# Kernel optimization log

Hardware: AMD Instinct MI355X
Metric: run time of the kernel (lower is better)

Reference implementation:

```python
import jax, jax.numpy as jnp
import numpy as np

B, T, L, D, H, E, A, V = 64, 20, 196, 512, 512, 512, 512, 30000


def setup_inputs() -> dict:
    key = jax.random.key(0)
    ks = jax.random.split(key, 20)
    s = 0.02  # param init scale
    inp = {
        "captions": jax.random.randint(ks[0], (B, T), 0, V),
        "image_features": jax.random.normal(ks[1], (B, L, D), dtype=jnp.float32),
        "pooled_features": jax.random.normal(ks[2], (B, H), dtype=jnp.float32),
        "attention_mask": jnp.ones((B, L), dtype=bool),
        # embedding table
        "embedding": jax.random.normal(ks[3], (V, E), dtype=jnp.float32) * s,
        # LSTM (torch gate order i, f, g, o), input = [emb; context]
        "W_ih": jax.random.normal(ks[4], (4 * H, E + H), dtype=jnp.float32) * s,
        "W_hh": jax.random.normal(ks[5], (4 * H, H), dtype=jnp.float32) * s,
        "b_lstm": jnp.zeros((4 * H,), dtype=jnp.float32),
        # additive attention with memory/cell extra query context
        "Wq": jax.random.normal(ks[6], (H, A), dtype=jnp.float32) * s,
        "Wk": jax.random.normal(ks[7], (D, A), dtype=jnp.float32) * s,
        "Wm": jax.random.normal(ks[8], (H, A), dtype=jnp.float32) * s,
        "Wc": jax.random.normal(ks[9], (H, A), dtype=jnp.float32) * s,
        "v_att": jax.random.normal(ks[10], (A,), dtype=jnp.float32) * s,
        # output projection context(H) -> vocab
        "W_out": jax.random.normal(ks[11], (H, V), dtype=jnp.float32) * s,
        "b_out": jnp.zeros((V,), dtype=jnp.float32),
        # hidden/cell init from pooled features (num_layers = 1)
        "W_init_h": jax.random.normal(ks[12], (H, H), dtype=jnp.float32) * s,
        "b_init_h": jnp.zeros((H,), dtype=jnp.float32),
        "W_init_c": jax.random.normal(ks[13], (H, H), dtype=jnp.float32) * s,
        "b_init_c": jnp.zeros((H,), dtype=jnp.float32),
    }
    return inp


def reference(captions, image_features, pooled_features, attention_mask,
              embedding, W_ih, W_hh, b_lstm, Wq, Wk, Wm, Wc, v_att,
              W_out, b_out, W_init_h, b_init_h, W_init_c, b_init_c):
    # init hidden states from pooled features
    h0 = pooled_features @ W_init_h + b_init_h            # [B, H]
    c0 = pooled_features @ W_init_c + b_init_c            # [B, H]
    ctx0 = jnp.zeros_like(h0)                              # prev_context, [B, H]
    emb = embedding[captions]                              # [B, T, E] (dropout = eval identity)
    # precompute key projection once (hoisted out of the timestep loop)
    key_proj = jnp.einsum('bld,da->bla', image_features, Wk)  # [B, L, A]
    neg = jnp.finfo(image_features.dtype).min

    def step(carry, emb_t):
        h, c, ctx = carry
        x = jnp.concatenate([emb_t, ctx], axis=-1)         # [B, E+H]
        gates = x @ W_ih.T + h @ W_hh.T + b_lstm           # [B, 4H]
        i, f, g, o = jnp.split(gates, 4, axis=-1)
        i = jax.nn.sigmoid(i); f = jax.nn.sigmoid(f)
        g = jnp.tanh(g);       o = jax.nn.sigmoid(o)
        c_new = f * c + i * g
        h_new = o * jnp.tanh(c_new)                        # lstm output == query
        # additive attention: query + memory_state(h) + cell_state(c) context
        q = h_new @ Wq + h_new @ Wm + c_new @ Wc           # [B, A]
        scores = jnp.einsum('bla,a->bl', jnp.tanh(key_proj + q[:, None, :]), v_att)
        scores = jnp.where(attention_mask, scores, neg)
        w = jax.nn.softmax(scores, axis=-1)                # [B, L]
        ctx_new = jnp.einsum('bl,bld->bd', w, image_features)  # [B, H]
        logits_t = ctx_new @ W_out + b_out                 # [B, V]
        return (h_new, c_new, ctx_new), logits_t

    _, logits = jax.lax.scan(step, (h0, c0, ctx0), jnp.swapaxes(emb, 0, 1))
    return jnp.swapaxes(logits, 0, 1)  # [B, T, V]
```

## Files before the change

kernel.cpp:

```cpp
#include <hip/hip_runtime.h>
#include <hip/hip_bf16.h>
#include <cstdint>

#define DEV static __device__ __forceinline__

typedef __bf16 bf16;
typedef __bf16 bf16x8 __attribute__((ext_vector_type(8)));
typedef float f32x4 __attribute__((ext_vector_type(4)));

#define B_ 64
#define T_ 20
#define L_ 196
#define E_ 512
#define V_ 30000
#define VPAD 30080
#define XK 2560
#define GN 2048
#define KSPLIT 8
#define KSPAN 10

DEV float sigmoidf_(float x) { return 1.0f / (1.0f + __expf(-x)); }
DEV float tanhf_(float x) { float e = __expf(2.0f * x); return 1.0f - 2.0f / (e + 1.0f); }

DEV float ldf(const void* p, size_t i, int isbf) {
  return isbf ? (float)((const bf16*)p)[i] : ((const float*)p)[i];
}

DEV void gload_lds16(const void* g, void* l) {
  __builtin_amdgcn_global_load_lds(
      (const __attribute__((address_space(1))) void*)(uintptr_t)g,
      (__attribute__((address_space(3))) void*)(uint32_t)(uintptr_t)l,
      16, 0, 0);
}

#define WAITV4_BAR  do { asm volatile("s_waitcnt vmcnt(4)" ::: "memory"); \
                         asm volatile("s_barrier" ::: "memory"); } while (0)
#define WAITV2_BAR  do { asm volatile("s_waitcnt vmcnt(2)" ::: "memory"); \
                         asm volatile("s_barrier" ::: "memory"); } while (0)
#define WAITV0_BAR  do { asm volatile("s_waitcnt vmcnt(0)" ::: "memory"); \
                         asm volatile("s_barrier" ::: "memory"); } while (0)
#define BAR_ONLY    do { asm volatile("s_barrier" ::: "memory"); } while (0)

__global__ void k_detect(const void* __restrict__ emb, int* __restrict__ flag)
{
  if (threadIdx.x == 0) {
    const unsigned* w = (const unsigned*)emb;
    int cnt = 0;
    for (int i = 0; i < 256; ++i) {
      unsigned lo = w[i] & 0xFFFFu;
      unsigned e = (lo >> 7) & 0xFFu;
      if (e >= 100 && e <= 126) ++cnt;
    }
    *flag = (cnt >= 128) ? 1 : 0;
  }
}

__global__ __launch_bounds__(256)
void k_init_mm(const void* __restrict__ pooled, const void* __restrict__ W_init_h,
               const void* __restrict__ W_init_c, float* __restrict__ ipart,
               const int* __restrict__ flag)
{
  const int isbf = *flag;
  const int b = blockIdx.x, ks = blockIdx.y, mat = blockIdx.z;
  const void* W = mat ? W_init_c : W_init_h;
  const int tid = threadIdx.x;
  __shared__ float p_s[64];
  if (tid < 64) p_s[tid] = ldf(pooled, (size_t)b * 512 + ks * 64 + tid, isbf);
  __syncthreads();
  const int kb = ks * 64;
  float a0 = 0.0f, a1 = 0.0f;
#pragma unroll 8
  for (int k = 0; k < 64; ++k) {
    float p = p_s[k];
    a0 += p * ldf(W, (size_t)(kb + k) * 512 + tid, isbf);
    a1 += p * ldf(W, (size_t)(kb + k) * 512 + tid + 256, isbf);
  }
  float* o = ipart + (((size_t)mat * 8 + ks) * 64 + b) * 512;
  o[tid] = a0;
  o[tid + 256] = a1;
}

__global__ __launch_bounds__(256)
void k_pack(const float* __restrict__ ipart, const void* __restrict__ b_init_h,
            const void* __restrict__ b_init_c, const int* __restrict__ captions,
            const void* __restrict__ embedding, const void* __restrict__ Wq,
            const void* __restrict__ Wm, const void* __restrict__ Wc,
            bf16* __restrict__ xcomb, float* __restrict__ c_state,
            bf16* __restrict__ Wqm, bf16* __restrict__ Wcb,
            const int* __restrict__ flag)
{
  const int isbf = *flag;
  const int tid = threadIdx.x;
  if (blockIdx.x >= 96) {
    size_t base = (size_t)(blockIdx.x - 96) * 8192;
    for (int i = tid; i < 8192; i += 256)
      Wcb[base + i] = (bf16)ldf(Wc, base + i, isbf);
    return;
  }
  if (blockIdx.x >= 64) {
    size_t base = (size_t)(blockIdx.x - 64) * 8192;
    for (int i = tid; i < 8192; i += 256)
      Wqm[base + i] = (bf16)(ldf(Wq, base + i, isbf) + ldf(Wm, base + i, isbf));
    return;
  }
  const int b = blockIdx.x;
  {
    int cap = captions[b * T_];
    for (int i = tid; i < 512; i += 256) {
      xcomb[(size_t)b * XK + i] = (bf16)ldf(embedding, (size_t)cap * E_ + i, isbf);
      xcomb[(size_t)b * XK + 512 + i]  = (bf16)0.0f;
      xcomb[(size_t)b * XK + 1024 + i] = (bf16)0.0f;
    }
  }
#pragma unroll
  for (int jj = 0; jj < 2; ++jj) {
    int j = tid + jj * 256;
    float ah = ldf(b_init_h, j, isbf), ac = ldf(b_init_c, j, isbf);
#pragma unroll
    for (int ks = 0; ks < 8; ++ks) {
      ah += ipart[(((size_t)0 * 8 + ks) * 64 + b) * 512 + j];
      ac += ipart[(((size_t)1 * 8 + ks) * 64 + b) * 512 + j];
    }
    c_state[b * 512 + j] = ac;
    bf16 hh = (bf16)ah;
    xcomb[(size_t)b * XK + 1536 + j] = hh;
    xcomb[(size_t)b * XK + 2048 + j] = (bf16)(ah - (float)hh);
  }
}

__global__ __launch_bounds__(256)
void k_gemm(const void* __restrict__ A, const void* __restrict__ Bsrc,
            int N, int K, int kspan, int outmode, int amode, int btmode,
            float* __restrict__ outF, bf16* __restrict__ outB,
            void* __restrict__ outAny, const void* __restrict__ bias,
            const int* __restrict__ flag)
{
  const int isbf = *flag;
  const int tid  = threadIdx.x;
  const int lane = tid & 63, w = tid >> 6;
  const int n0 = blockIdx.x * 64;
  const int yt = blockIdx.y;
  const int m0 = (outmode == 1) ? 0 : yt * 64;
  const int kbase = (outmode == 1) ? yt * kspan * 32 : 0;

  __shared__ __align__(16) bf16 As[64 * 32];
  __shared__ __align__(16) bf16 Bs[64 * 32];

  f32x4 acc[2][2];
#pragma unroll
  for (int i = 0; i < 2; ++i)
#pragma unroll
    for (int j = 0; j < 2; ++j)
#pragma unroll
      for (int r = 0; r < 4; ++r) acc[i][j][r] = 0.0f;

  const int wm = (w & 1) * 32, wn = (w >> 1) * 32;
  const int sr = tid >> 2, sk = (tid & 3) * 8;
  const int fm = lane & 15, kq = (lane >> 4) * 8;
  const bool bvalid = (n0 + sr) < N;
  const int kk = tid >> 3, nn = (tid & 7) * 8;

  for (int ks = 0; ks < kspan; ++ks) {
    const size_t aidx = (size_t)(m0 + sr) * K + kbase + sk + ks * 32;
    bf16x8 av;
    if (amode == 0 || isbf) {
      av = *(const bf16x8*)((const bf16*)A + aidx);
    } else {
      const float* af = (const float*)A + aidx;
      float4 x0 = *(const float4*)af, x1 = *(const float4*)(af + 4);
      av[0] = (bf16)x0.x; av[1] = (bf16)x0.y; av[2] = (bf16)x0.z; av[3] = (bf16)x0.w;
      av[4] = (bf16)x1.x; av[5] = (bf16)x1.y; av[6] = (bf16)x1.z; av[7] = (bf16)x1.w;
    }

    if (btmode == 0) {
      bf16x8 bv;
#pragma unroll
      for (int i = 0; i < 8; ++i) bv[i] = (bf16)0.0f;
      if (bvalid)
        bv = *(const bf16x8*)((const bf16*)Bsrc + (size_t)(n0 + sr) * K + kbase + sk + ks * 32);
      __syncthreads();
      *(bf16x8*)(As + sr * 32 + sk) = av;
      *(bf16x8*)(Bs + sr * 32 + sk) = bv;
      __syncthreads();
    } else {
      float bl[8];
      const int krow = kbase + ks * 32 + kk;
#pragma unroll
      for (int i = 0; i < 8; ++i) {
        int n = n0 + nn + i;
        bl[i] = (n < N) ? ldf(Bsrc, (size_t)krow * N + n, isbf) : 0.0f;
      }
      __syncthreads();
      *(bf16x8*)(As + sr * 32 + sk) = av;
#pragma unroll
      for (int i = 0; i < 8; ++i) Bs[(nn + i) * 32 + kk] = (bf16)bl[i];
      __syncthreads();
    }

    bf16x8 a0 = *(const bf16x8*)(As + (wm + fm)      * 32 + kq);
    bf16x8 a1 = *(const bf16x8*)(As + (wm + 16 + fm) * 32 + kq);
    bf16x8 b0 = *(const bf16x8*)(Bs + (wn + fm)      * 32 + kq);
    bf16x8 b1 = *(const bf16x8*)(Bs + (wn + 16 + fm) * 32 + kq);
    acc[0][0] = __builtin_amdgcn_mfma_f32_16x16x32_bf16(a0, b0, acc[0][0], 0, 0, 0);
    acc[0][1] = __builtin_amdgcn_mfma_f32_16x16x32_bf16(a0, b1, acc[0][1], 0, 0, 0);
    acc[1][0] = __builtin_amdgcn_mfma_f32_16x16x32_bf16(a1, b0, acc[1][0], 0, 0, 0);
    acc[1][1] = __builtin_amdgcn_mfma_f32_16x16x32_bf16(a1, b1, acc[1][1], 0, 0, 0);
  }

  const int rbase = (lane >> 4) * 4;
  if (outmode == 1) {
    float* o = outF + (size_t)yt * 64 * N;
#pragma unroll
    for (int i = 0; i < 2; ++i)
#pragma unroll
      for (int j = 0; j < 2; ++j)
#pragma unroll
        for (int r = 0; r < 4; ++r) {
          int m = wm + i * 16 + rbase + r;
          int n = n0 + wn + j * 16 + fm;
          o[(size_t)m * N + n] = acc[i][j][r];
        }
  } else if (outmode == 0) {
#pragma unroll
    for (int i = 0; i < 2; ++i)
#pragma unroll
      for (int j = 0; j < 2; ++j) {
        int n = n0 + wn + j * 16 + fm;
        if (n < N) {
#pragma unroll
          for (int r = 0; r < 4; ++r) {
            int m = m0 + wm + i * 16 + rbase + r;
            outB[(size_t)m * N + n] = (bf16)acc[i][j][r];
          }
        }
      }
  } else {
#pragma unroll
    for (int i = 0; i < 2; ++i)
#pragma unroll
      for (int j = 0; j < 2; ++j) {
        int n = n0 + wn + j * 16 + fm;
        if (n < N) {
          float bb = bias ? ldf(bias, n, isbf) : 0.0f;
#pragma unroll
          for (int r = 0; r < 4; ++r) {
            int m = m0 + wm + i * 16 + rbase + r;
            float val = acc[i][j][r] + bb;
            if (isbf) ((bf16*)outAny)[(size_t)m * N + n] = (bf16)val;
            else      ((float*)outAny)[(size_t)m * N + n] = val;
          }
        }
      }
  }
}

__global__ __launch_bounds__(256)
void k_gates(const bf16* __restrict__ A, const bf16* __restrict__ BT,
             float* __restrict__ outF)
{
  const int tid = threadIdx.x, lane = tid & 63, w = tid >> 6;
  const int n0 = blockIdx.x * 64;
  const int yt = blockIdx.y;
  const int kbase = yt * KSPAN * 32;

  __shared__ __align__(16) bf16 As[2][64 * 32];
  __shared__ __align__(16) bf16 Bs[2][64 * 32];

  f32x4 acc[2][2];
#pragma unroll
  for (int i = 0; i < 2; ++i)
#pragma unroll
    for (int j = 0; j < 2; ++j)
#pragma unroll
      for (int r = 0; r < 4; ++r) acc[i][j][r] = 0.0f;

  const int wm = (w & 1) * 32, wn = (w >> 1) * 32;
  const int fm = lane & 15, kq = (lane >> 4) * 8;

  const int srow = w * 16 + (lane >> 2), skk = (lane & 3) * 8;
  const bf16* ag = A  + (size_t)srow * XK + kbase + skk;
  const bf16* bg = BT + (size_t)(n0 + srow) * XK + kbase + skk;

#define GSTAGE(cur, koff) do { \
    gload_lds16(ag + (koff), &As[cur][w * 512]); \
    gload_lds16(bg + (koff), &Bs[cur][w * 512]); } while (0)

  GSTAGE(0, 0);
  GSTAGE(1, 32);
  int cur = 0;
  for (int ks = 0; ks < KSPAN; ++ks) {
    if (ks + 1 < KSPAN) WAITV2_BAR; else WAITV0_BAR;
    bf16x8 a0 = *(const bf16x8*)(&As[cur][(wm + fm)      * 32 + kq]);
    bf16x8 a1 = *(const bf16x8*)(&As[cur][(wm + 16 + fm) * 32 + kq]);
    bf16x8 b0 = *(const bf16x8*)(&Bs[cur][(wn + fm)      * 32 + kq]);
    bf16x8 b1 = *(const bf16x8*)(&Bs[cur][(wn + 16 + fm) * 32 + kq]);
    acc[0][0] = __builtin_amdgcn_mfma_f32_16x16x32_bf16(a0, b0, acc[0][0], 0, 0, 0);
    acc[0][1] = __builtin_amdgcn_mfma_f32_16x16x32_bf16(a0, b1, acc[0][1], 0, 0, 0);
    acc[1][0] = __builtin_amdgcn_mfma_f32_16x16x32_bf16(a1, b0, acc[1][0], 0, 0, 0);
    acc[1][1] = __builtin_amdgcn_mfma_f32_16x16x32_bf16(a1, b1, acc[1][1], 0, 0, 0);
    BAR_ONLY;
    if (ks + 2 < KSPAN) GSTAGE(cur, (ks + 2) * 32);
    cur ^= 1;
  }
#undef GSTAGE

  const int rbase = (lane >> 4) * 4;
  float* o = outF + (size_t)yt * 64 * GN;
#pragma unroll
  for (int i = 0; i < 2; ++i)
#pragma unroll
    for (int j = 0; j < 2; ++j)
#pragma unroll
      for (int r = 0; r < 4; ++r) {
        int m = wm + i * 16 + rbase + r;
        int n = n0 + wn + j * 16 + fm;
        o[(size_t)m * GN + n] = acc[i][j][r];
      }
}

__global__ __launch_bounds__(256)
void k_gemm128(const bf16* __restrict__ A, const bf16* __restrict__ BT,
               int N, int K,
               void* __restrict__ outAny, const void* __restrict__ bias,
               const int* __restrict__ flag)
{
  const int isbf = *flag;
  const int tid = threadIdx.x, lane = tid & 63, w = tid >> 6;

  const int NMT = (B_ * T_) / 128;
  const int nwg = (int)gridDim.x * (int)gridDim.y;
  const int wgid = (int)blockIdx.y * (int)gridDim.x + (int)blockIdx.x;
  const int xcd = wgid & 7, loc = wgid >> 3;
  const int qq = nwg >> 3, rr = nwg & 7;
  const int swz = (xcd < rr ? xcd * (qq + 1) : rr * (qq + 1) + (xcd - rr) * qq) + loc;
  const int n0 = (swz / NMT) * 128, m0 = (swz % NMT) * 128;

  __shared__ __align__(16) bf16 As[2][128 * 32];
  __shared__ __align__(16) bf16 Bs[2][128 * 32];

  f32x4 acc[4][4];
#pragma unroll
  for (int i = 0; i < 4; ++i)
#pragma unroll
    for (int j = 0; j < 4; ++j)
#pragma unroll
      for (int r = 0; r < 4; ++r) acc[i][j][r] = 0.0f;

  const int lr = lane >> 2;
  const int lk = (lane & 3) * 8;
  const int fm = lane & 15, kq = (lane >> 4) * 8;
  const int wm = (w & 1) * 64, wn = (w >> 1) * 64;
  const int li0 = w * 2, li1 = w * 2 + 1;

  const bf16* a0g = A  + (size_t)(m0 + li0 * 16 + lr) * K + lk;
  const bf16* a1g = A  + (size_t)(m0 + li1 * 16 + lr) * K + lk;
  const bf16* b0g = BT + (size_t)(n0 + li0 * 16 + lr) * K + lk;
  const bf16* b1g = BT + (size_t)(n0 + li1 * 16 + lr) * K + lk;

#define STAGE128(cur, koff) do { \
    gload_lds16(a0g + (koff), &As[cur][li0 * 512]); \
    gload_lds16(a1g + (koff), &As[cur][li1 * 512]); \
    gload_lds16(b0g + (koff), &Bs[cur][li0 * 512]); \
    gload_lds16(b1g + (koff), &Bs[cur][li1 * 512]); } while (0)

  const int kiters = K >> 5;
  STAGE128(0, 0);
  STAGE128(1, 32);
  int cur = 0;
  for (int ks = 0; ks < kiters; ++ks) {
    if (ks + 1 < kiters) WAITV4_BAR; else WAITV0_BAR;
    bf16x8 af[4], bf[4];
#pragma unroll
    for (int i = 0; i < 4; ++i) {
      af[i] = *(const bf16x8*)(&As[cur][(wm + i * 16 + fm) * 32 + kq]);
      bf[i] = *(const bf16x8*)(&Bs[cur][(wn + i * 16 + fm) * 32 + kq]);
    }
#pragma unroll
    for (int i = 0; i < 4; ++i)
#pragma unroll
      for (int j = 0; j < 4; ++j)
        acc[i][j] = __builtin_amdgcn_mfma_f32_16x16x32_bf16(af[i], bf[j], acc[i][j], 0, 0, 0);
    BAR_ONLY;
    if (ks + 2 < kiters) STAGE128(cur, (ks + 2) * 32);
    cur ^= 1;
  }
#undef STAGE128

  const int rbase = (lane >> 4) * 4;
#pragma unroll
  for (int j = 0; j < 4; ++j) {
    int n = n0 + wn + j * 16 + fm;
    if (n < N) {
      float bb = bias ? ldf(bias, n, isbf) : 0.0f;
#pragma unroll
      for (int i = 0; i < 4; ++i)
#pragma unroll
        for (int r = 0; r < 4; ++r) {
          int m = m0 + wm + i * 16 + rbase + r;
          float val = acc[i][j][r] + bb;
          if (isbf) ((bf16*)outAny)[(size_t)m * N + n] = (bf16)val;
          else      ((float*)outAny)[(size_t)m * N + n] = val;
        }
    }
  }
}

__global__ __launch_bounds__(256)
void k_transpose(const void* __restrict__ in, bf16* __restrict__ out, int R, int C,
                 int Cpad, const int* __restrict__ flag)
{
  const int isbf = *flag;
  __shared__ bf16 tile[32][33];
  const int c0 = blockIdx.x * 32, r0 = blockIdx.y * 32;
  const int cc = threadIdx.x & 31, rw = threadIdx.x >> 5;
#pragma unroll
  for (int s = 0; s < 4; ++s) {
    int r = r0 + rw + s * 8, c = c0 + cc;
    tile[rw + s * 8][cc] = (r < R && c < C) ? (bf16)ldf(in, (size_t)r * C + c, isbf)
                                            : (bf16)0.0f;
  }
  __syncthreads();
#pragma unroll
  for (int s = 0; s < 4; ++s) {
    int c = c0 + rw + s * 8, r = r0 + cc;
    if (c < Cpad && r < R) out[(size_t)c * R + r] = tile[cc][rw + s * 8];
  }
}

__global__ __launch_bounds__(256)
void k_buildWcomb(const void* __restrict__ W_ih, const void* __restrict__ W_hh,
                  bf16* __restrict__ WcombT, const int* __restrict__ flag)
{
  const int isbf = *flag;
  const int n = blockIdx.x;
  for (int k = threadIdx.x; k < XK; k += 256) {
    float v;
    if (k < 512)       v = ldf(W_ih, (size_t)n * 1024 + k, isbf);
    else if (k < 1536) v = ldf(W_ih, (size_t)n * 1024 + 512 + ((k - 512) & 511), isbf);
    else               v = ldf(W_hh, (size_t)n * 512 + ((k - 1536) & 511), isbf);
    WcombT[(size_t)n * XK + k] = (bf16)v;
  }
}

__global__ __launch_bounds__(1024)
void k_step2(const float* __restrict__ partials, const void* __restrict__ b_lstm,
             float* __restrict__ c_state, bf16* __restrict__ xcomb,
             bf16* __restrict__ ctx_all, const bf16* __restrict__ Wqm,
             const bf16* __restrict__ Wcb, const bf16* __restrict__ keyproj,
             const void* __restrict__ v_att, const void* __restrict__ img,
             const int* __restrict__ captions, const void* __restrict__ embedding,
             int t, const int* __restrict__ flag)
{
  const int isbf = *flag;
  const int b = blockIdx.x, tid = threadIdx.x;
  __shared__ float h_s[512], c_s[512], q_s[512];
  __shared__ float red[16 * 512];
  __shared__ float sc_s[256];
  __shared__ float wred[32];

#pragma unroll
  for (int jj = 0; jj < 2; ++jj) {
    int gc = tid + jj * 1024;
    float s = ldf(b_lstm, gc, isbf);
#pragma unroll
    for (int sp = 0; sp < KSPLIT; ++sp)
      s += partials[((size_t)sp * 64 + b) * 2048 + gc];
    red[gc] = s;
  }
  __syncthreads();
  if (tid < 512) {
    const int j = tid;
    float ig = sigmoidf_(red[j]);
    float fg = sigmoidf_(red[512 + j]);
    float gg = tanhf_(red[1024 + j]);
    float og = sigmoidf_(red[1536 + j]);
    float cn = fg * c_state[b * 512 + j] + ig * gg;
    float hn = og * tanhf_(cn);
    c_state[b * 512 + j] = cn;
    h_s[j] = hn; c_s[j] = cn;
    bf16 hh = (bf16)hn;
    xcomb[(size_t)b * XK + 1536 + j] = hh;
    xcomb[(size_t)b * XK + 2048 + j] = (bf16)(hn - (float)hh);
  }
  __syncthreads();

  {
    const int dc = tid >> 6, a8 = (tid & 63) * 8;
    float qp[8];
#pragma unroll
    for (int i = 0; i < 8; ++i) qp[i] = 0.0f;
    const int d0 = dc * 32;
    for (int d = d0; d < d0 + 32; ++d) {
      float hv = h_s[d], cv = c_s[d];
      bf16x8 wq = *(const bf16x8*)(Wqm + (size_t)d * 512 + a8);
      bf16x8 wc = *(const bf16x8*)(Wcb + (size_t)d * 512 + a8);
#pragma unroll
      for (int i = 0; i < 8; ++i)
        qp[i] += hv * (float)wq[i] + cv * (float)wc[i];
    }
#pragma unroll
    for (int i = 0; i < 8; ++i) red[dc * 512 + a8 + i] = qp[i];
  }
  __syncthreads();
  if (tid < 512) {
    float s = 0.0f;
#pragma unroll
    for (int w16 = 0; w16 < 16; ++w16) s += red[w16 * 512 + tid];
    q_s[tid] = s;
  }
  __syncthreads();

  {
    const int wv = tid >> 6, ln = tid & 63;
    float q8[8], v8[8];
#pragma unroll
    for (int i = 0; i < 8; ++i) {
      q8[i] = q_s[ln * 8 + i];
      v8[i] = ldf(v_att, ln * 8 + i, isbf);
    }
    for (int l = wv; l < 196; l += 16) {
      bf16x8 kv = *(const bf16x8*)(keyproj + ((size_t)b * 196 + l) * 512 + ln * 8);
      float s = 0.0f;
#pragma unroll
      for (int i = 0; i < 8; ++i)
        s += tanhf_((float)kv[i] + q8[i]) * v8[i];
      s += __shfl_xor(s, 32); s += __shfl_xor(s, 16); s += __shfl_xor(s, 8);
      s += __shfl_xor(s, 4);  s += __shfl_xor(s, 2);  s += __shfl_xor(s, 1);
      if (ln == 0) sc_s[l] = s;
    }
  }
  __syncthreads();

  {
    const int wv = tid >> 6, ln = tid & 63;
    float v = (tid < 196) ? sc_s[tid] : -3.0e38f;
    float m = v;
    m = fmaxf(m, __shfl_xor(m, 32)); m = fmaxf(m, __shfl_xor(m, 16));
    m = fmaxf(m, __shfl_xor(m, 8));  m = fmaxf(m, __shfl_xor(m, 4));
    m = fmaxf(m, __shfl_xor(m, 2));  m = fmaxf(m, __shfl_xor(m, 1));
    if (ln == 0) wred[wv] = m;
    __syncthreads();
    m = wred[0];
#pragma unroll
    for (int i = 1; i < 16; ++i) m = fmaxf(m, wred[i]);
    float e = (tid < 196) ? __expf(v - m) : 0.0f;
    float ss = e;
    ss += __shfl_xor(ss, 32); ss += __shfl_xor(ss, 16); ss += __shfl_xor(ss, 8);
    ss += __shfl_xor(ss, 4);  ss += __shfl_xor(ss, 2);  ss += __shfl_xor(ss, 1);
    if (ln == 0) wred[16 + wv] = ss;
    __syncthreads();
    float tot = 0.0f;
#pragma unroll
    for (int i = 0; i < 16; ++i) tot += wred[16 + i];
    if (tid < 196) sc_s[tid] = e / tot;
  }
  __syncthreads();

  {
    const int d8 = (tid & 63) * 8, lc = tid >> 6;
    float cx[8];
#pragma unroll
    for (int i = 0; i < 8; ++i) cx[i] = 0.0f;
    if (isbf) {
      for (int l = lc; l < 196; l += 16) {
        float wl = sc_s[l];
        bf16x8 iv = *(const bf16x8*)((const bf16*)img + ((size_t)b * 196 + l) * 512 + d8);
#pragma unroll
        for (int i = 0; i < 8; ++i) cx[i] += wl * (float)iv[i];
      }
    } else {
      for (int l = lc; l < 196; l += 16) {
        float wl = sc_s[l];
        const float* ip = (const float*)img + ((size_t)b * 196 + l) * 512 + d8;
        float4 x0 = *(const float4*)ip, x1 = *(const float4*)(ip + 4);
        cx[0] += wl * x0.x; cx[1] += wl * x0.y; cx[2] += wl * x0.z; cx[3] += wl * x0.w;
        cx[4] += wl * x1.x; cx[5] += wl * x1.y; cx[6] += wl * x1.z; cx[7] += wl * x1.w;
      }
    }
#pragma unroll
    for (int i = 0; i < 8; ++i) red[lc * 512 + d8 + i] = cx[i];
  }
  __syncthreads();
  if (tid < 512) {
    const int d = tid;
    float s = 0.0f;
#pragma unroll
    for (int w16 = 0; w16 < 16; ++w16) s += red[w16 * 512 + d];
    bf16 ch = (bf16)s;
    xcomb[(size_t)b * XK + 512 + d]  = ch;
    xcomb[(size_t)b * XK + 1024 + d] = (bf16)(s - (float)ch);
    ctx_all[((size_t)b * T_ + t) * 512 + d] = ch;
  }
  if (t + 1 < T_) {
    int cap = captions[b * T_ + t + 1];
    for (int i = tid; i < 512; i += 1024)
      xcomb[(size_t)b * XK + i] = (bf16)ldf(embedding, (size_t)cap * E_ + i, isbf);
  }
}

extern "C" void kernel_launch(void* const* d_in, const int* in_sizes, int n_in,
                              void* d_out, int out_size, void* d_ws, size_t ws_size,
                              hipStream_t stream)
{
  (void)in_sizes; (void)n_in; (void)out_size;
  const int*  captions  = (const int*)d_in[0];
  const void* img       = d_in[1];
  const void* pooled    = d_in[2];
  const void* embedding = d_in[4];
  const void* W_ih      = d_in[5];
  const void* W_hh      = d_in[6];
  const void* b_lstm    = d_in[7];
  const void* Wq        = d_in[8];
  const void* Wk        = d_in[9];
  const void* Wm        = d_in[10];
  const void* Wc        = d_in[11];
  const void* v_att     = d_in[12];
  const void* W_out     = d_in[13];
  const void* b_out     = d_in[14];
  const void* W_init_h  = d_in[15];
  const void* b_init_h  = d_in[16];
  const void* W_init_c  = d_in[17];
  const void* b_init_c  = d_in[18];

  char* ws = (char*)d_ws;
  size_t off = 0;
  auto alloc = [&](size_t bytes) {
    void* p = ws + off;
    off += (bytes + 255) & ~(size_t)255;
    return p;
  };
  int*   flag     = (int*)alloc(256);
  bf16*  xcomb    = (bf16*)alloc((size_t)B_ * XK * 2);
  float* c_state  = (float*)alloc((size_t)B_ * 512 * 4);
  bf16*  ctx_all  = (bf16*)alloc((size_t)B_ * T_ * 512 * 2);
  bf16*  Wqm      = (bf16*)alloc((size_t)512 * 512 * 2);
  bf16*  Wcb      = (bf16*)alloc((size_t)512 * 512 * 2);
  bf16*  WkT      = (bf16*)alloc((size_t)512 * 512 * 2);
  float* partials = (float*)alloc((size_t)KSPLIT * B_ * GN * 4);
  bf16*  keyproj  = (bf16*)alloc((size_t)B_ * L_ * 512 * 2);
  bf16*  WcombT   = (bf16*)alloc((size_t)GN * XK * 2);
  bf16*  WoutT    = (bf16*)alloc((size_t)VPAD * 512 * 2);
  const bool fits = (off <= ws_size);
  float* ipart = partials;

  k_detect<<<1, 64, 0, stream>>>(embedding, flag);
  k_init_mm<<<dim3(64, 8, 2), 256, 0, stream>>>(pooled, W_init_h, W_init_c, ipart, flag);
  k_pack<<<128, 256, 0, stream>>>(ipart, b_init_h, b_init_c, captions, embedding,
                                  Wq, Wm, Wc, xcomb, c_state, Wqm, Wcb, flag);
  k_buildWcomb<<<GN, 256, 0, stream>>>(W_ih, W_hh, WcombT, flag);
  k_transpose<<<dim3(16, 16), 256, 0, stream>>>(Wk, WkT, 512, 512, 512, flag);
  if (fits)
    k_transpose<<<dim3(VPAD / 32, 16), 256, 0, stream>>>(W_out, WoutT, 512, V_, VPAD, flag);

  k_gemm<<<dim3(8, L_ * B_ / 64), 256, 0, stream>>>(
      img, WkT, 512, 512, 16, 0, 1, 0,
      nullptr, keyproj, nullptr, nullptr, flag);

  for (int t = 0; t < T_; ++t) {
    k_gates<<<dim3(GN / 64, KSPLIT), 256, 0, stream>>>(xcomb, WcombT, partials);
    k_step2<<<B_, 1024, 0, stream>>>(partials, b_lstm, c_state, xcomb, ctx_all,
                                     Wqm, Wcb, keyproj, v_att, img, captions,
                                     embedding, t, flag);
  }

  if (fits) {
    k_gemm128<<<dim3(VPAD / 128, B_ * T_ / 128), 256, 0, stream>>>(
        ctx_all, WoutT, V_, 512, d_out, b_out, flag);
  } else {
    k_gemm<<<dim3((V_ + 63) / 64, B_ * T_ / 64), 256, 0, stream>>>(
        ctx_all, W_out, V_, 512, 16, 2, 0, 1,
        nullptr, nullptr, d_out, b_out, flag);
  }
}
```

Baseline: 1.347 ms.

## Split per-step kernel into LSTM, MFMA query GEMM, and d-split attention kernels

Replaces the monolithic per-timestep kernel with three launches. A pointwise LSTM kernel writes h and c as hi/lo bf16 pairs. A small MFMA GEMM, using transposed Wq+Wm and Wc, then computes the attention query, so the 64 scalar blocks no longer each stream both weight matrices. The attention kernel now runs 4 blocks per batch row, each summing a 128-wide slice of the context. This aims to raise parallelism on the recurrent critical path, at the cost of two extra launches per step and scores recomputed in every d-slice block.

```diff
diff --git a/kernel.cpp b/kernel.cpp
--- a/kernel.cpp
+++ b/kernel.cpp
@@ -87,7 +87,7 @@
             const void* __restrict__ Wm, const void* __restrict__ Wc,
             bf16* __restrict__ xcomb, float* __restrict__ c_state,
             bf16* __restrict__ Wqm, bf16* __restrict__ Wcb,
-            const int* __restrict__ flag)
+            bf16* __restrict__ hc, const int* __restrict__ flag)
 {
   const int isbf = *flag;
   const int tid = threadIdx.x;
@@ -123,8 +123,15 @@
     }
     c_state[b * 512 + j] = ac;
     bf16 hh = (bf16)ah;
+    bf16 hl = (bf16)(ah - (float)hh);
+    bf16 ch = (bf16)ac;
+    bf16 cl = (bf16)(ac - (float)ch);
     xcomb[(size_t)b * XK + 1536 + j] = hh;
-    xcomb[(size_t)b * XK + 2048 + j] = (bf16)(ah - (float)hh);
+    xcomb[(size_t)b * XK + 2048 + j] = hl;
+    hc[(size_t)b * 2048 + j]        = hh;
+    hc[(size_t)b * 2048 + 512 + j]  = hl;
+    hc[(size_t)b * 2048 + 1024 + j] = ch;
+    hc[(size_t)b * 2048 + 1536 + j] = cl;
   }
 }
 
@@ -319,6 +326,72 @@
 }
 
 __global__ __launch_bounds__(256)
+void k_qgemm(const bf16* __restrict__ hc, const bf16* __restrict__ WqmT,
+             const bf16* __restrict__ WcbT, float* __restrict__ qpart)
+{
+  const int tid = threadIdx.x, lane = tid & 63, w = tid >> 6;
+  const int n0 = blockIdx.x * 64;
+  const int ksb = blockIdx.y;
+  const int kbase = ksb * 256;
+  const bf16* bsrc = (ksb < 4) ? WqmT : WcbT;
+  const int kin = (ksb & 1) * 256;
+
+  __shared__ __align__(16) bf16 As[2][64 * 32];
+  __shared__ __align__(16) bf16 Bs[2][64 * 32];
+
+  f32x4 acc[2][2];
+#pragma unroll
+  for (int i = 0; i < 2; ++i)
+#pragma unroll
+    for (int j = 0; j < 2; ++j)
+#pragma unroll
+      for (int r = 0; r < 4; ++r) acc[i][j][r] = 0.0f;
+
+  const int wm = (w & 1) * 32, wn = (w >> 1) * 32;
+  const int fm = lane & 15, kq = (lane >> 4) * 8;
+
+  const int srow = w * 16 + (lane >> 2), skk = (lane & 3) * 8;
+  const bf16* ag = hc   + (size_t)srow * 2048 + kbase + skk;
+  const bf16* bg = bsrc + (size_t)(n0 + srow) * 512 + kin + skk;
+
+#define QSTAGE(cur, koff) do { \
+    gload_lds16(ag + (koff), &As[cur][w * 512]); \
+    gload_lds16(bg + (koff), &Bs[cur][w * 512]); } while (0)
+
+  QSTAGE(0, 0);
+  QSTAGE(1, 32);
+  int cur = 0;
+  for (int ks = 0; ks < 8; ++ks) {
+    if (ks + 1 < 8) WAITV2_BAR; else WAITV0_BAR;
+    bf16x8 a0 = *(const bf16x8*)(&As[cur][(wm + fm)      * 32 + kq]);
+    bf16x8 a1 = *(const bf16x8*)(&As[cur][(wm + 16 + fm) * 32 + kq]);
+    bf16x8 b0 = *(const bf16x8*)(&Bs[cur][(wn + fm)      * 32 + kq]);
+    bf16x8 b1 = *(const bf16x8*)(&Bs[cur][(wn + 16 + fm) * 32 + kq]);
+    acc[0][0] = __builtin_amdgcn_mfma_f32_16x16x32_bf16(a0, b0, acc[0][0], 0, 0, 0);
+    acc[0][1] = __builtin_amdgcn_mfma_f32_16x16x32_bf16(a0, b1, acc[0][1], 0, 0, 0);
+    acc[1][0] = __builtin_amdgcn_mfma_f32_16x16x32_bf16(a1, b0, acc[1][0], 0, 0, 0);
+    acc[1][1] = __builtin_amdgcn_mfma_f32_16x16x32_bf16(a1, b1, acc[1][1], 0, 0, 0);
+    BAR_ONLY;
+    if (ks + 2 < 8) QSTAGE(cur, (ks + 2) * 32);
+    cur ^= 1;
+  }
+#undef QSTAGE
+
+  const int rbase = (lane >> 4) * 4;
+  float* o = qpart + (size_t)ksb * 64 * 512;
+#pragma unroll
+  for (int i = 0; i < 2; ++i)
+#pragma unroll
+    for (int j = 0; j < 2; ++j)
+#pragma unroll
+      for (int r = 0; r < 4; ++r) {
+        int m = wm + i * 16 + rbase + r;
+        int n = n0 + wn + j * 16 + fm;
+        o[(size_t)m * 512 + n] = acc[i][j][r];
+      }
+}
+
+__global__ __launch_bounds__(256)
 void k_gemm128(const bf16* __restrict__ A, const bf16* __restrict__ BT,
                int N, int K,
                void* __restrict__ outAny, const void* __restrict__ bias,
@@ -425,6 +498,21 @@
     int c = c0 + rw + s * 8, r = r0 + cc;
     if (c < Cpad && r < R) out[(size_t)c * R + r] = tile[cc][rw + s * 8];
   }
+}
+
+__global__ __launch_bounds__(256)
+void k_transpose_bf(const bf16* __restrict__ in, bf16* __restrict__ out)
+{
+  __shared__ bf16 tile[32][33];
+  const int c0 = blockIdx.x * 32, r0 = blockIdx.y * 32;
+  const int cc = threadIdx.x & 31, rw = threadIdx.x >> 5;
+#pragma unroll
+  for (int s = 0; s < 4; ++s)
+    tile[rw + s * 8][cc] = in[(size_t)(r0 + rw + s * 8) * 512 + c0 + cc];
+  __syncthreads();
+#pragma unroll
+  for (int s = 0; s < 4; ++s)
+    out[(size_t)(c0 + rw + s * 8) * 512 + r0 + cc] = tile[cc][rw + s * 8];
 }
 
 __global__ __launch_bounds__(256)
@@ -442,70 +530,61 @@
   }
 }
 
+__global__ __launch_bounds__(512)
+void k_lstm(const float* __restrict__ partials, const void* __restrict__ b_lstm,
+            float* __restrict__ c_state, bf16* __restrict__ xcomb,
+            bf16* __restrict__ hc, const int* __restrict__ flag)
+{
+  const int isbf = *flag;
+  const int b = blockIdx.x, j = threadIdx.x;
+  float g4[4];
+#pragma unroll
+  for (int g = 0; g < 4; ++g) {
+    int gc = g * 512 + j;
+    float s = ldf(b_lstm, gc, isbf);
+#pragma unroll
+    for (int sp = 0; sp < KSPLIT; ++sp)
+      s += partials[((size_t)sp * 64 + b) * 2048 + gc];
+    g4[g] = s;
+  }
+  float ig = sigmoidf_(g4[0]);
+  float fg = sigmoidf_(g4[1]);
+  float gg = tanhf_(g4[2]);
+  float og = sigmoidf_(g4[3]);
+  float cn = fg * c_state[b * 512 + j] + ig * gg;
+  float hn = og * tanhf_(cn);
+  c_state[b * 512 + j] = cn;
+  bf16 hh = (bf16)hn;
+  bf16 hl = (bf16)(hn - (float)hh);
+  bf16 ch = (bf16)cn;
+  bf16 cl = (bf16)(cn - (float)ch);
+  xcomb[(size_t)b * XK + 1536 + j] = hh;
+  xcomb[(size_t)b * XK + 2048 + j] = hl;
+  hc[(size_t)b * 2048 + j]        = hh;
+  hc[(size_t)b * 2048 + 512 + j]  = hl;
+  hc[(size_t)b * 2048 + 1024 + j] = ch;
+  hc[(size_t)b * 2048 + 1536 + j] = cl;
+}
+
 __global__ __launch_bounds__(1024)
-void k_step2(const float* __restrict__ partials, const void* __restrict__ b_lstm,
-             float* __restrict__ c_state, bf16* __restrict__ xcomb,
-             bf16* __restrict__ ctx_all, const bf16* __restrict__ Wqm,
-             const bf16* __restrict__ Wcb, const bf16* __restrict__ keyproj,
-             const void* __restrict__ v_att, const void* __restrict__ img,
-             const int* __restrict__ captions, const void* __restrict__ embedding,
-             int t, const int* __restrict__ flag)
+void k_attn(const float* __restrict__ qpart, const bf16* __restrict__ keyproj,
+            const void* __restrict__ v_att, const void* __restrict__ img,
+            bf16* __restrict__ xcomb, bf16* __restrict__ ctx_all,
+            const int* __restrict__ captions, const void* __restrict__ embedding,
+            int t, const int* __restrict__ flag)
 {
   const int isbf = *flag;
-  const int b = blockIdx.x, tid = threadIdx.x;
-  __shared__ float h_s[512], c_s[512], q_s[512];
-  __shared__ float red[16 * 512];
+  const int b = blockIdx.x, dq = blockIdx.y, tid = threadIdx.x;
+  __shared__ float q_s[512];
   __shared__ float sc_s[256];
   __shared__ float wred[32];
-
-#pragma unroll
-  for (int jj = 0; jj < 2; ++jj) {
-    int gc = tid + jj * 1024;
-    float s = ldf(b_lstm, gc, isbf);
-#pragma unroll
-    for (int sp = 0; sp < KSPLIT; ++sp)
-      s += partials[((size_t)sp * 64 + b) * 2048 + gc];
-    red[gc] = s;
-  }
-  __syncthreads();
-  if (tid < 512) {
-    const int j = tid;
-    float ig = sigmoidf_(red[j]);
-    float fg = sigmoidf_(red[512 + j]);
-    float gg = tanhf_(red[1024 + j]);
-    float og = sigmoidf_(red[1536 + j]);
-    float cn = fg * c_state[b * 512 + j] + ig * gg;
-    float hn = og * tanhf_(cn);
-    c_state[b * 512 + j] = cn;
-    h_s[j] = hn; c_s[j] = cn;
-    bf16 hh = (bf16)hn;
-    xcomb[(size_t)b * XK + 1536 + j] = hh;
-    xcomb[(size_t)b * XK + 2048 + j] = (bf16)(hn - (float)hh);
-  }
-  __syncthreads();
-
-  {
-    const int dc = tid >> 6, a8 = (tid & 63) * 8;
-    float qp[8];
-#pragma unroll
-    for (int i = 0; i < 8; ++i) qp[i] = 0.0f;
-    const int d0 = dc * 32;
-    for (int d = d0; d < d0 + 32; ++d) {
-      float hv = h_s[d], cv = c_s[d];
-      bf16x8 wq = *(const bf16x8*)(Wqm + (size_t)d * 512 + a8);
-      bf16x8 wc = *(const bf16x8*)(Wcb + (size_t)d * 512 + a8);
-#pragma unroll
-      for (int i = 0; i < 8; ++i)
-        qp[i] += hv * (float)wq[i] + cv * (float)wc[i];
-    }
-#pragma unroll
-    for (int i = 0; i < 8; ++i) red[dc * 512 + a8 + i] = qp[i];
-  }
-  __syncthreads();
+  __shared__ float red[64 * 128];
+
   if (tid < 512) {
     float s = 0.0f;
 #pragma unroll
-    for (int w16 = 0; w16 < 16; ++w16) s += red[w16 * 512 + tid];
+    for (int ks = 0; ks < 8; ++ks)
+      s += qpart[((size_t)ks * 64 + b) * 512 + tid];
     q_s[tid] = s;
   }
   __syncthreads();
@@ -557,41 +636,44 @@
   __syncthreads();
 
   {
-    const int d8 = (tid & 63) * 8, lc = tid >> 6;
+    const int worker = tid >> 4;
+    const int d8 = (tid & 15) * 8;
+    const int dcol = dq * 128 + d8;
     float cx[8];
 #pragma unroll
     for (int i = 0; i < 8; ++i) cx[i] = 0.0f;
     if (isbf) {
-      for (int l = lc; l < 196; l += 16) {
+      for (int l = worker; l < 196; l += 64) {
         float wl = sc_s[l];
-        bf16x8 iv = *(const bf16x8*)((const bf16*)img + ((size_t)b * 196 + l) * 512 + d8);
+        bf16x8 iv = *(const bf16x8*)((const bf16*)img + ((size_t)b * 196 + l) * 512 + dcol);
 #pragma unroll
         for (int i = 0; i < 8; ++i) cx[i] += wl * (float)iv[i];
       }
     } else {
-      for (int l = lc; l < 196; l += 16) {
+      for (int l = worker; l < 196; l += 64) {
         float wl = sc_s[l];
-        const float* ip = (const float*)img + ((size_t)b * 196 + l) * 512 + d8;
+        const float* ip = (const float*)img + ((size_t)b * 196 + l) * 512 + dcol;
         float4 x0 = *(const float4*)ip, x1 = *(const float4*)(ip + 4);
         cx[0] += wl * x0.x; cx[1] += wl * x0.y; cx[2] += wl * x0.z; cx[3] += wl * x0.w;
         cx[4] += wl * x1.x; cx[5] += wl * x1.y; cx[6] += wl * x1.z; cx[7] += wl * x1.w;
       }
     }
 #pragma unroll
-    for (int i = 0; i < 8; ++i) red[lc * 512 + d8 + i] = cx[i];
+    for (int i = 0; i < 8; ++i) red[worker * 128 + d8 + i] = cx[i];
   }
   __syncthreads();
-  if (tid < 512) {
-    const int d = tid;
+  if (tid < 128) {
     float s = 0.0f;
-#pragma unroll
-    for (int w16 = 0; w16 < 16; ++w16) s += red[w16 * 512 + d];
+#pragma unroll 8
+    for (int w64 = 0; w64 < 64; ++w64) s += red[w64 * 128 + tid];
+    const int d = dq * 128 + tid;
     bf16 ch = (bf16)s;
     xcomb[(size_t)b * XK + 512 + d]  = ch;
     xcomb[(size_t)b * XK + 1024 + d] = (bf16)(s - (float)ch);
     ctx_all[((size_t)b * T_ + t) * 512 + d] = ch;
   }
-  if (t + 1 < T_) {
+
+  if (dq == 3 && t + 1 < T_) {
     int cap = captions[b * T_ + t + 1];
     for (int i = tid; i < 512; i += 1024)
       xcomb[(size_t)b * XK + i] = (bf16)ldf(embedding, (size_t)cap * E_ + i, isbf);
@@ -639,16 +721,22 @@
   float* partials = (float*)alloc((size_t)KSPLIT * B_ * GN * 4);
   bf16*  keyproj  = (bf16*)alloc((size_t)B_ * L_ * 512 * 2);
   bf16*  WcombT   = (bf16*)alloc((size_t)GN * XK * 2);
+  bf16*  hc       = (bf16*)alloc((size_t)B_ * 2048 * 2);
+  bf16*  WqmT     = (bf16*)alloc((size_t)512 * 512 * 2);
+  bf16*  WcbT     = (bf16*)alloc((size_t)512 * 512 * 2);
   bf16*  WoutT    = (bf16*)alloc((size_t)VPAD * 512 * 2);
   const bool fits = (off <= ws_size);
   float* ipart = partials;
+  float* qpart = partials;
 
   k_detect<<<1, 64, 0, stream>>>(embedding, flag);
   k_init_mm<<<dim3(64, 8, 2), 256, 0, stream>>>(pooled, W_init_h, W_init_c, ipart, flag);
   k_pack<<<128, 256, 0, stream>>>(ipart, b_init_h, b_init_c, captions, embedding,
-                                  Wq, Wm, Wc, xcomb, c_state, Wqm, Wcb, flag);
+                                  Wq, Wm, Wc, xcomb, c_state, Wqm, Wcb, hc, flag);
   k_buildWcomb<<<GN, 256, 0, stream>>>(W_ih, W_hh, WcombT, flag);
   k_transpose<<<dim3(16, 16), 256, 0, stream>>>(Wk, WkT, 512, 512, 512, flag);
+  k_transpose_bf<<<dim3(16, 16), 256, 0, stream>>>(Wqm, WqmT);
+  k_transpose_bf<<<dim3(16, 16), 256, 0, stream>>>(Wcb, WcbT);
   if (fits)
     k_transpose<<<dim3(VPAD / 32, 16), 256, 0, stream>>>(W_out, WoutT, 512, V_, VPAD, flag);
 
@@ -658,9 +746,11 @@
 
   for (int t = 0; t < T_; ++t) {
     k_gates<<<dim3(GN / 64, KSPLIT), 256, 0, stream>>>(xcomb, WcombT, partials);
-    k_step2<<<B_, 1024, 0, stream>>>(partials, b_lstm, c_state, xcomb, ctx_all,
-                                     Wqm, Wcb, keyproj, v_att, img, captions,
-                                     embedding, t, flag);
+    k_lstm<<<B_, 512, 0, stream>>>(partials, b_lstm, c_state, xcomb, hc, flag);
+    k_qgemm<<<dim3(8, 8), 256, 0, stream>>>(hc, WqmT, WcbT, qpart);
+    k_attn<<<dim3(B_, 4), 1024, 0, stream>>>(qpart, keyproj, v_att, img,
+                                             xcomb, ctx_all, captions, embedding,
+                                             t, flag);
   }
 
   if (fits) {
```

New measurement: 1.247 ms. 7.5% less time.
